# Kernel tuning notes

Measured on AMD Instinct MI355X. Metric: run time of the kernel, lower is better.

Reference implementation:

```python
import jax, jax.numpy as jnp
import numpy as np
from itertools import combinations

ADD = 3  # matches init_kwargs

def setup_inputs() -> dict:
    key = jax.random.key(0)
    x = jax.random.uniform(key, (131072, 16), dtype=jnp.float32)
    return {"x": x}

def reference(x) -> jnp.ndarray:
    n = x.shape[1]
    parts = [x]
    for i in range(2, ADD + 1):
        # static index table of all size-i column subsets: [C(n,i), i]
        idx = jnp.asarray(np.array(list(combinations(range(n), i)), dtype=np.int32))
        # gather + reduce: x[:, idx] -> [N, C, i]; Lukasiewicz t-norm = max(sum - (i-1), 0)
        s = jnp.sum(x[:, idx], axis=2)  # [N, C]
        parts.append(jnp.maximum(s - jnp.float32(i - 1), jnp.float32(0)))
    return jnp.concatenate(parts, axis=1)
```

## Files before the change

kernel.cpp:

```cpp
#include <hip/hip_runtime.h>
#include <hip/hip_bf16.h>


#define NCOLS 696
#define ROWS_PER_BLOCK 256
#define CHUNK_COLS 24
#define CHUNK_QUADS 6
#define NCHUNKS 29
#define LDS_STRIDE_Q 7

typedef float v4f __attribute__((ext_vector_type(4)));

struct Tabs { short a[NCOLS]; short b[NCOLS]; short c[NCOLS]; };

constexpr Tabs make_tabs() {
    Tabs t{};
    int k = 0;
    for (int a = 0; a < 16; ++a) { t.a[k] = (short)a; t.b[k] = -1; t.c[k] = -1; ++k; }
    for (int a = 0; a < 16; ++a)
        for (int b = a + 1; b < 16; ++b) { t.a[k] = (short)a; t.b[k] = (short)b; t.c[k] = -1; ++k; }
    for (int a = 0; a < 16; ++a)
        for (int b = a + 1; b < 16; ++b)
            for (int c = b + 1; c < 16; ++c) { t.a[k] = (short)a; t.b[k] = (short)b; t.c[k] = (short)c; ++k; }
    return t;
}
constexpr Tabs TT = make_tabs();

__device__ __forceinline__ float colval(const float (&xv)[16], int cc) {
    const int a = TT.a[cc], b = TT.b[cc], c = TT.c[cc];
    if (b < 0) return xv[a];
    if (c < 0) return fmaxf(xv[a] + xv[b] - 1.0f, 0.0f);
    return fmaxf(xv[a] + xv[b] + xv[c] - 2.0f, 0.0f);
}

__global__ __launch_bounds__(256, 2)
void luk_kernel(const float* __restrict__ x, float* __restrict__ out) {
    __shared__ v4f lds[ROWS_PER_BLOCK * LDS_STRIDE_Q];

    const int t    = threadIdx.x;
    const int wave = t >> 6;
    const int lane = t & 63;
    const size_t row = (size_t)blockIdx.x * ROWS_PER_BLOCK + t;

    float xv[16];
    {
        const v4f* __restrict__ xr = reinterpret_cast<const v4f*>(x + row * 16);
        #pragma unroll
        for (int j = 0; j < 4; ++j) {
            const v4f v = xr[j];
            xv[4 * j + 0] = v.x; xv[4 * j + 1] = v.y;
            xv[4 * j + 2] = v.z; xv[4 * j + 3] = v.w;
        }
    }

    v4f* const myw   = &lds[t * LDS_STRIDE_Q];
    v4f* const rbase = &lds[(wave << 6) * LDS_STRIDE_Q];
    float* const wout = out + ((size_t)blockIdx.x * ROWS_PER_BLOCK + (wave << 6)) * NCOLS;

    #pragma unroll
    for (int ch = 0; ch < NCHUNKS; ++ch) {
        const int c0 = ch * CHUNK_COLS;

        #pragma unroll
        for (int q = 0; q < CHUNK_QUADS; ++q) {
            v4f o;
            o.x = colval(xv, c0 + 4 * q + 0);
            o.y = colval(xv, c0 + 4 * q + 1);
            o.z = colval(xv, c0 + 4 * q + 2);
            o.w = colval(xv, c0 + 4 * q + 3);
            myw[q] = o;
        }
        __threadfence_block();

        #pragma unroll
        for (int v = 0; v < CHUNK_QUADS; ++v) {
            const unsigned g = (unsigned)(v * 64 + lane);
            const unsigned r = g / 6u;
            const unsigned q = g - r * 6u;
            const v4f val = rbase[r * LDS_STRIDE_Q + q];
            *reinterpret_cast<v4f*>(wout + (size_t)r * NCOLS + (c0 + 4 * q)) = val;
        }
        __threadfence_block();
    }
}

extern "C" void kernel_launch(void* const* d_in, const int* in_sizes, int n_in,
                              void* d_out, int out_size, void* d_ws, size_t ws_size,
                              hipStream_t stream) {
    const float* x = (const float*)d_in[0];
    float* out = (float*)d_out;
    const int nrows  = in_sizes[0] / 16;
    const int blocks = nrows / ROWS_PER_BLOCK;
    luk_kernel<<<blocks, 256, 0, stream>>>(x, out);
}
```

Before: 445.8 us.

## Widen LDS staging chunks to 64 columns and use lgkmcnt fences

Each row's output is now staged through LDS in 64-column chunks (11 chunks, the last holding 56 columns) instead of 24-column chunks. The write-out maps 16 lanes per row so each group of lanes stores a contiguous 256-byte segment. The __threadfence_block calls are replaced by an inline s_waitcnt lgkmcnt(0). The aim is longer contiguous global stores and fewer chunk iterations, at the cost of much more LDS per block (about 70KB), which may limit occupancy. The lane mask also leaves some lanes idle in the last chunk.

```diff
diff --git a/kernel.cpp b/kernel.cpp
--- a/kernel.cpp
+++ b/kernel.cpp
@@ -4,10 +4,8 @@
 
 #define NCOLS 696
 #define ROWS_PER_BLOCK 256
-#define CHUNK_COLS 24
-#define CHUNK_QUADS 6
-#define NCHUNKS 29
-#define LDS_STRIDE_Q 7
+#define STRIDE_Q 17
+#define NCHUNKS 11
 
 typedef float v4f __attribute__((ext_vector_type(4)));
 
@@ -33,9 +31,13 @@
     return fmaxf(xv[a] + xv[b] + xv[c] - 2.0f, 0.0f);
 }
 
+__device__ __forceinline__ void lgkm_fence() {
+    __asm__ volatile("s_waitcnt lgkmcnt(0)" ::: "memory");
+}
+
 __global__ __launch_bounds__(256, 2)
 void luk_kernel(const float* __restrict__ x, float* __restrict__ out) {
-    __shared__ v4f lds[ROWS_PER_BLOCK * LDS_STRIDE_Q];
+    __shared__ v4f lds[ROWS_PER_BLOCK * STRIDE_Q];
 
     const int t    = threadIdx.x;
     const int wave = t >> 6;
@@ -53,16 +55,18 @@
         }
     }
 
-    v4f* const myw   = &lds[t * LDS_STRIDE_Q];
-    v4f* const rbase = &lds[(wave << 6) * LDS_STRIDE_Q];
-    float* const wout = out + ((size_t)blockIdx.x * ROWS_PER_BLOCK + (wave << 6)) * NCOLS;
+    v4f* const myw  = &lds[t * STRIDE_Q];
+    const v4f* const rb = &lds[(wave << 6) * STRIDE_Q];
+    float* const wbase = out +
+        ((size_t)blockIdx.x * ROWS_PER_BLOCK + (size_t)(wave << 6)) * NCOLS;
 
     #pragma unroll
     for (int ch = 0; ch < NCHUNKS; ++ch) {
-        const int c0 = ch * CHUNK_COLS;
+        const int Q  = (ch == NCHUNKS - 1) ? 14 : 16;
+        const int c0 = ch * 64;
 
         #pragma unroll
-        for (int q = 0; q < CHUNK_QUADS; ++q) {
+        for (int q = 0; q < Q; ++q) {
             v4f o;
             o.x = colval(xv, c0 + 4 * q + 0);
             o.y = colval(xv, c0 + 4 * q + 1);
@@ -70,17 +74,18 @@
             o.w = colval(xv, c0 + 4 * q + 3);
             myw[q] = o;
         }
-        __threadfence_block();
+        lgkm_fence();
 
         #pragma unroll
-        for (int v = 0; v < CHUNK_QUADS; ++v) {
-            const unsigned g = (unsigned)(v * 64 + lane);
-            const unsigned r = g / 6u;
-            const unsigned q = g - r * 6u;
-            const v4f val = rbase[r * LDS_STRIDE_Q + q];
-            *reinterpret_cast<v4f*>(wout + (size_t)r * NCOLS + (c0 + 4 * q)) = val;
+        for (int i = 0; i < 16; ++i) {
+            const int r = 4 * i + (lane >> 4);
+            const int q = lane & 15;
+            if (q < Q) {
+                const v4f val = rb[r * STRIDE_Q + q];
+                *reinterpret_cast<v4f*>(wbase + (size_t)r * NCOLS + c0 + 4 * q) = val;
+            }
         }
-        __threadfence_block();
+        lgkm_fence();
     }
 }
 
```

Measured after the change: 447.1 us. About the same (+0.3%).
